# Kernel optimization log

Measured on AMD Instinct MI355X. Metric: run time of the kernel, lower is better.

## Reference

```python
import jax, jax.numpy as jnp
import numpy as np

B, C, H, W = 256, 2048, 16, 8
NUM_CLASSES = 10000
SCALE = 1.0  # cls_layer.s for cls_type='Linear', scale=1
N_ITERS = 20


def setup_inputs() -> dict:
    key = jax.random.key(0)
    k1, k2, k3 = jax.random.split(key, 3)
    features = jax.random.normal(k1, (B, C, H, W), dtype=jnp.float32)
    targets = jax.random.randint(k2, (B,), 0, NUM_CLASSES)
    # nn.init.normal_(self.weight, std=0.01)
    weight = jax.random.normal(k3, (NUM_CLASSES, C), dtype=jnp.float32) * 0.01
    return {"features": features, "targets": targets, "weight": weight}


def reference(features, targets, weight):
    # 1) GlobalAvgPool over H,W then squeeze -> [B, C]; bottleneck is identity
    #    (embedding_dim=0, with_bnneck=False).
    neck_feat = features.mean(axis=(2, 3))
    t = neck_feat.shape[0]

    # cls_type == 'Linear': logits = F.linear(neck_feat, weight); cls_layer is
    # a pass-through, so every loop iteration computes identical quantities
    # (the random 'maskarea' in the original is overwritten before use).
    logits = jnp.einsum('bc,nc->bn', neck_feat, weight)  # [B, num_classes]
    soft = jax.nn.softmax(logits, axis=1)

    # right_prob = softmax probability at the target class (scatter+mul+sum)
    right_prob = jnp.take_along_axis(soft, targets[:, None], axis=1)[:, 0]  # [t]

    # All N_ITERS iterations append the same right_prob, so at the final
    # iteration: mean == right_prob, variance over iterations == 0.
    mean_sl = right_prob                      # [t]
    var_sl = jnp.zeros_like(right_prob)       # [t]
    con = mean_sl / (var_sl * 1e4)            # -> +inf (matches torch div-by-0)
    ri = jnp.tanh(1.2 * con)                  # tanh(inf) = 1.0
    # new_weight[i] = t * ri[i] / ri.sum()
    new_weight = (t * ri / ri.sum())[None, :]  # [1, t]

    cls_outputs = logits                       # Linear cls layer is identity
    pred_class_logits = logits * SCALE
    feat = neck_feat                           # neck_feat == 'before', bottleneck identity
    return cls_outputs, pred_class_logits, feat, new_weight
```

## Files before the change

kernel.cpp:

```cpp
#include <hip/hip_runtime.h>


#define OUT1_OFF (256 * 10000)
#define FEAT_OFF (2 * 256 * 10000)
#define NW_OFF   (2 * 256 * 10000 + 256 * 2048)

typedef __attribute__((ext_vector_type(4))) float f32x4;
typedef __attribute__((ext_vector_type(8))) short bf16x8;
typedef __attribute__((ext_vector_type(4))) unsigned int u32x4;

__device__ inline unsigned pk2bf(float lo, float hi) {
    unsigned a = __float_as_uint(lo), b = __float_as_uint(hi);
    unsigned ra = (a + 0x7FFFu + ((a >> 16) & 1u)) >> 16;
    unsigned rb = (b + 0x7FFFu + ((b >> 16) & 1u)) & 0xFFFF0000u;
    return ra | rb;
}

__device__ inline void gload_lds16(const void* g, void* l) {
    __builtin_amdgcn_global_load_lds(
        (const __attribute__((address_space(1))) void*)g,
        (__attribute__((address_space(3))) void*)l, 16, 0, 0);
}

__global__ __launch_bounds__(256) void pool_kernel(
    const float* __restrict__ f, float* __restrict__ out,
    unsigned int* __restrict__ wsA32) {
    int tid = threadIdx.x;
    int g = tid >> 5;
    int l = tid & 31;
    int r0 = blockIdx.x * 16 + g * 2;
    const f32x4* s0 = (const f32x4*)(f + (size_t)r0 * 128);
    f32x4 v0 = s0[l];
    f32x4 v1 = s0[l + 32];
    float a = v0[0] + v0[1] + v0[2] + v0[3];
    float b = v1[0] + v1[1] + v1[2] + v1[3];
#pragma unroll
    for (int off = 16; off >= 1; off >>= 1) {
        a += __shfl_xor(a, off);
        b += __shfl_xor(b, off);
    }
    if (l == 0) {
        float m0 = a * (1.0f / 128.0f), m1 = b * (1.0f / 128.0f);
        float2 fv; fv.x = m0; fv.y = m1;
        *(float2*)&out[FEAT_OFF + r0] = fv;
        int bb = r0 >> 11, c = r0 & 2047;
        int chunk = ((bb >> 4) * 256 + (c >> 3)) * 16 + (bb & 15);
        wsA32[chunk * 4 + ((c & 7) >> 1)] = pk2bf(m0, m1);
    }
    if (blockIdx.x == 0) out[NW_OFF + tid] = 1.0f;
}

__global__ __launch_bounds__(512) void gemm_kernel(
    const u32x4* __restrict__ A16, const float* __restrict__ W,
    float* __restrict__ out) {
    __shared__ u32x4 As[3][2048];
    __shared__ u32x4 Bs[3][512];

    int tid = threadIdx.x;
    int n0 = blockIdx.x * 64;
    int wid = tid >> 6, lane = tid & 63;
    int wm = wid >> 1, wn = wid & 1;
    int r = lane & 15, kqu = lane >> 4;

    const u32x4* ga[4];
#pragma unroll
    for (int i = 0; i < 4; ++i) {
        int ci = tid + i * 512;
        ga[i] = A16 + (((ci >> 7) * 256 + ((ci >> 4) & 7)) * 16 + (ci & 15));
    }
    int nr = n0 + (((tid >> 7) << 4) | (tid & 15));
    if (nr > 9999) nr = 9999;
    int kg = (tid >> 4) & 7;
    const f32x4* gb = (const f32x4*)(W + (size_t)nr * 2048 + kg * 8);

    f32x4 acc[4][2];
#pragma unroll
    for (int i = 0; i < 4; ++i)
#pragma unroll
        for (int j = 0; j < 2; ++j) acc[i][j] = (f32x4){0.f, 0.f, 0.f, 0.f};

    f32x4 rbA0, rbA1, rbB0, rbB1;

#define STAGE_A(kt, buf)                                           \
    {                                                              \
        _Pragma("unroll") for (int i = 0; i < 4; ++i)              \
            gload_lds16(ga[i] + (kt) * 128, &As[buf][tid + i * 512]); \
    }
#define LOAD_B(kt, r0_, r1_)                \
    {                                       \
        r0_ = gb[(kt) * 16];                \
        r1_ = gb[(kt) * 16 + 1];            \
    }
#define PACK_B(buf, r0_, r1_)                              \
    {                                                      \
        u32x4 p;                                           \
        p.x = pk2bf(r0_[0], r0_[1]);                       \
        p.y = pk2bf(r0_[2], r0_[3]);                       \
        p.z = pk2bf(r1_[0], r1_[1]);                       \
        p.w = pk2bf(r1_[2], r1_[3]);                       \
        Bs[buf][tid] = p;                                  \
    }

    STAGE_A(0, 0); LOAD_B(0, rbA0, rbA1);
    STAGE_A(1, 1); LOAD_B(1, rbB0, rbB1);
    asm volatile("s_waitcnt vmcnt(6)" ::: "memory");
    __builtin_amdgcn_sched_barrier(0);
    PACK_B(0, rbA0, rbA1);
    asm volatile("s_waitcnt lgkmcnt(0)" ::: "memory");
    __builtin_amdgcn_sched_barrier(0);
    __builtin_amdgcn_s_barrier();
    __builtin_amdgcn_sched_barrier(0);

    for (int kt = 0; kt < 32; ++kt) {
        int cur = kt % 3;
        if (kt <= 29) {
            int nx2 = (kt + 2) % 3;
            STAGE_A(kt + 2, nx2);
            if (kt & 1) { LOAD_B(kt + 2, rbB0, rbB1); }
            else        { LOAD_B(kt + 2, rbA0, rbA1); }
        }
#pragma unroll
        for (int ks = 0; ks < 2; ++ks) {
            int kcl = ks * 4 + kqu;
            bf16x8 av[4], bv[2];
#pragma unroll
            for (int i = 0; i < 4; ++i)
                av[i] = *(const bf16x8*)&As[cur][(wm * 4 + i) * 128 + kcl * 16 + r];
#pragma unroll
            for (int j = 0; j < 2; ++j)
                bv[j] = *(const bf16x8*)&Bs[cur][(wn * 2 + j) * 128 + kcl * 16 + r];
#pragma unroll
            for (int i = 0; i < 4; ++i)
#pragma unroll
                for (int j = 0; j < 2; ++j)
                    acc[i][j] = __builtin_amdgcn_mfma_f32_16x16x32_bf16(
                        av[i], bv[j], acc[i][j], 0, 0, 0);
        }
        if (kt <= 29) { asm volatile("s_waitcnt vmcnt(6)" ::: "memory"); }
        else          { asm volatile("s_waitcnt vmcnt(0)" ::: "memory"); }
        __builtin_amdgcn_sched_barrier(0);
        if (kt <= 30) {
            int nx1 = (kt + 1) % 3;
            if (kt & 1) { PACK_B(nx1, rbA0, rbA1); }
            else        { PACK_B(nx1, rbB0, rbB1); }
            asm volatile("s_waitcnt lgkmcnt(0)" ::: "memory");
            __builtin_amdgcn_sched_barrier(0);
            __builtin_amdgcn_s_barrier();
        }
        __builtin_amdgcn_sched_barrier(0);
    }

#pragma unroll
    for (int i = 0; i < 4; ++i)
#pragma unroll
        for (int j = 0; j < 2; ++j) {
            int n = n0 + (wn * 2 + j) * 16 + r;
            if (n < 10000) {
                int mbase = (wm * 4 + i) * 16 + kqu * 4;
#pragma unroll
                for (int q = 0; q < 4; ++q) {
                    float v = acc[i][j][q];
                    size_t off = (size_t)(mbase + q) * 10000 + n;
                    out[off] = v;
                    out[OUT1_OFF + off] = v;
                }
            }
        }
#undef STAGE_A
#undef LOAD_B
#undef PACK_B
}

extern "C" void kernel_launch(void* const* d_in, const int* in_sizes, int n_in,
                              void* d_out, int out_size, void* d_ws, size_t ws_size,
                              hipStream_t stream) {
    const float* feats = (const float*)d_in[0];
    const float* weight = (const float*)d_in[2];
    float* out = (float*)d_out;

    pool_kernel<<<32768, 256, 0, stream>>>(feats, out, (unsigned int*)d_ws);
    gemm_kernel<<<157, 512, 0, stream>>>((const u32x4*)d_ws, weight, out);
}
```

Before: 105.0 us.

## Split GEMM across M halves and coarsen pooling work per block

The GEMM grid now splits the 256-row M dimension into two halves, launching 314 blocks instead of 157 so more CUs on the device get work. Each block keeps a smaller A tile and fewer accumulators, at the cost of reading and bf16-converting the weight matrix twice. The pooling kernel now handles 256 rows per block over 8 iterations with 4 rows per group, using vectorized stores, which cuts the block count from 32768 to 2048.

```diff
diff --git a/kernel.cpp b/kernel.cpp
--- a/kernel.cpp
+++ b/kernel.cpp
@@ -28,24 +28,37 @@
     int tid = threadIdx.x;
     int g = tid >> 5;
     int l = tid & 31;
-    int r0 = blockIdx.x * 16 + g * 2;
-    const f32x4* s0 = (const f32x4*)(f + (size_t)r0 * 128);
-    f32x4 v0 = s0[l];
-    f32x4 v1 = s0[l + 32];
-    float a = v0[0] + v0[1] + v0[2] + v0[3];
-    float b = v1[0] + v1[1] + v1[2] + v1[3];
 #pragma unroll
-    for (int off = 16; off >= 1; off >>= 1) {
-        a += __shfl_xor(a, off);
-        b += __shfl_xor(b, off);
-    }
-    if (l == 0) {
-        float m0 = a * (1.0f / 128.0f), m1 = b * (1.0f / 128.0f);
-        float2 fv; fv.x = m0; fv.y = m1;
-        *(float2*)&out[FEAT_OFF + r0] = fv;
-        int bb = r0 >> 11, c = r0 & 2047;
-        int chunk = ((bb >> 4) * 256 + (c >> 3)) * 16 + (bb & 15);
-        wsA32[chunk * 4 + ((c & 7) >> 1)] = pk2bf(m0, m1);
+    for (int it = 0; it < 8; ++it) {
+        int r0 = blockIdx.x * 256 + it * 32 + g * 4;
+        const f32x4* s0 = (const f32x4*)(f + (size_t)r0 * 128);
+        f32x4 v0 = s0[l];
+        f32x4 v1 = s0[l + 32];
+        f32x4 v2 = s0[l + 64];
+        f32x4 v3 = s0[l + 96];
+        float a0 = v0[0] + v0[1] + v0[2] + v0[3];
+        float a1 = v1[0] + v1[1] + v1[2] + v1[3];
+        float a2 = v2[0] + v2[1] + v2[2] + v2[3];
+        float a3 = v3[0] + v3[1] + v3[2] + v3[3];
+#pragma unroll
+        for (int off = 16; off >= 1; off >>= 1) {
+            a0 += __shfl_xor(a0, off);
+            a1 += __shfl_xor(a1, off);
+            a2 += __shfl_xor(a2, off);
+            a3 += __shfl_xor(a3, off);
+        }
+        if (l == 0) {
+            float m0 = a0 * (1.0f / 128.0f), m1 = a1 * (1.0f / 128.0f);
+            float m2 = a2 * (1.0f / 128.0f), m3 = a3 * (1.0f / 128.0f);
+            f32x4 fv = {m0, m1, m2, m3};
+            *(f32x4*)&out[FEAT_OFF + r0] = fv;
+            int bb = r0 >> 11, c = r0 & 2047;
+            int chunk = ((bb >> 4) * 256 + (c >> 3)) * 16 + (bb & 15);
+            uint2 pw;
+            pw.x = pk2bf(m0, m1);
+            pw.y = pk2bf(m2, m3);
+            *(uint2*)&wsA32[chunk * 4 + ((c & 7) >> 1)] = pw;
+        }
     }
     if (blockIdx.x == 0) out[NW_OFF + tid] = 1.0f;
 }
@@ -53,57 +66,58 @@
 __global__ __launch_bounds__(512) void gemm_kernel(
     const u32x4* __restrict__ A16, const float* __restrict__ W,
     float* __restrict__ out) {
-    __shared__ u32x4 As[3][2048];
+    __shared__ u32x4 As[3][1024];
     __shared__ u32x4 Bs[3][512];
 
     int tid = threadIdx.x;
-    int n0 = blockIdx.x * 64;
+    int mhalf = blockIdx.x;
+    int n0 = blockIdx.y * 64;
     int wid = tid >> 6, lane = tid & 63;
     int wm = wid >> 1, wn = wid & 1;
     int r = lane & 15, kqu = lane >> 4;
 
-    const u32x4* ga[4];
+    const u32x4* ga[2];
 #pragma unroll
-    for (int i = 0; i < 4; ++i) {
+    for (int i = 0; i < 2; ++i) {
         int ci = tid + i * 512;
-        ga[i] = A16 + (((ci >> 7) * 256 + ((ci >> 4) & 7)) * 16 + (ci & 15));
+        ga[i] = A16 + (((mhalf * 8 + (ci >> 7)) * 256 + ((ci >> 4) & 7)) * 16 + (ci & 15));
     }
     int nr = n0 + (((tid >> 7) << 4) | (tid & 15));
     if (nr > 9999) nr = 9999;
     int kg = (tid >> 4) & 7;
     const f32x4* gb = (const f32x4*)(W + (size_t)nr * 2048 + kg * 8);
 
-    f32x4 acc[4][2];
+    f32x4 acc[2][2];
 #pragma unroll
-    for (int i = 0; i < 4; ++i)
+    for (int i = 0; i < 2; ++i)
 #pragma unroll
         for (int j = 0; j < 2; ++j) acc[i][j] = (f32x4){0.f, 0.f, 0.f, 0.f};
 
     f32x4 rbA0, rbA1, rbB0, rbB1;
 
-#define STAGE_A(kt, buf)                                           \
-    {                                                              \
-        _Pragma("unroll") for (int i = 0; i < 4; ++i)              \
+#define STAGE_A(kt, buf)                                              \
+    {                                                                 \
+        _Pragma("unroll") for (int i = 0; i < 2; ++i)                 \
             gload_lds16(ga[i] + (kt) * 128, &As[buf][tid + i * 512]); \
     }
-#define LOAD_B(kt, r0_, r1_)                \
-    {                                       \
-        r0_ = gb[(kt) * 16];                \
-        r1_ = gb[(kt) * 16 + 1];            \
+#define LOAD_B(kt, r0_, r1_)     \
+    {                            \
+        r0_ = gb[(kt) * 16];     \
+        r1_ = gb[(kt) * 16 + 1]; \
     }
-#define PACK_B(buf, r0_, r1_)                              \
-    {                                                      \
-        u32x4 p;                                           \
-        p.x = pk2bf(r0_[0], r0_[1]);                       \
-        p.y = pk2bf(r0_[2], r0_[3]);                       \
-        p.z = pk2bf(r1_[0], r1_[1]);                       \
-        p.w = pk2bf(r1_[2], r1_[3]);                       \
-        Bs[buf][tid] = p;                                  \
+#define PACK_B(buf, r0_, r1_)            \
+    {                                    \
+        u32x4 p;                         \
+        p.x = pk2bf(r0_[0], r0_[1]);     \
+        p.y = pk2bf(r0_[2], r0_[3]);     \
+        p.z = pk2bf(r1_[0], r1_[1]);     \
+        p.w = pk2bf(r1_[2], r1_[3]);     \
+        Bs[buf][tid] = p;                \
     }
 
     STAGE_A(0, 0); LOAD_B(0, rbA0, rbA1);
     STAGE_A(1, 1); LOAD_B(1, rbB0, rbB1);
-    asm volatile("s_waitcnt vmcnt(6)" ::: "memory");
+    asm volatile("s_waitcnt vmcnt(4)" ::: "memory");
     __builtin_amdgcn_sched_barrier(0);
     PACK_B(0, rbA0, rbA1);
     asm volatile("s_waitcnt lgkmcnt(0)" ::: "memory");
@@ -122,21 +136,21 @@
 #pragma unroll
         for (int ks = 0; ks < 2; ++ks) {
             int kcl = ks * 4 + kqu;
-            bf16x8 av[4], bv[2];
+            bf16x8 av[2], bv[2];
 #pragma unroll
-            for (int i = 0; i < 4; ++i)
-                av[i] = *(const bf16x8*)&As[cur][(wm * 4 + i) * 128 + kcl * 16 + r];
+            for (int i = 0; i < 2; ++i)
+                av[i] = *(const bf16x8*)&As[cur][(wm * 2 + i) * 128 + kcl * 16 + r];
 #pragma unroll
             for (int j = 0; j < 2; ++j)
                 bv[j] = *(const bf16x8*)&Bs[cur][(wn * 2 + j) * 128 + kcl * 16 + r];
 #pragma unroll
-            for (int i = 0; i < 4; ++i)
+            for (int i = 0; i < 2; ++i)
 #pragma unroll
                 for (int j = 0; j < 2; ++j)
                     acc[i][j] = __builtin_amdgcn_mfma_f32_16x16x32_bf16(
                         av[i], bv[j], acc[i][j], 0, 0, 0);
         }
-        if (kt <= 29) { asm volatile("s_waitcnt vmcnt(6)" ::: "memory"); }
+        if (kt <= 29) { asm volatile("s_waitcnt vmcnt(4)" ::: "memory"); }
         else          { asm volatile("s_waitcnt vmcnt(0)" ::: "memory"); }
         __builtin_amdgcn_sched_barrier(0);
         if (kt <= 30) {
@@ -151,12 +165,12 @@
     }
 
 #pragma unroll
-    for (int i = 0; i < 4; ++i)
+    for (int i = 0; i < 2; ++i)
 #pragma unroll
         for (int j = 0; j < 2; ++j) {
             int n = n0 + (wn * 2 + j) * 16 + r;
             if (n < 10000) {
-                int mbase = (wm * 4 + i) * 16 + kqu * 4;
+                int mbase = mhalf * 128 + (wm * 2 + i) * 16 + kqu * 4;
 #pragma unroll
                 for (int q = 0; q < 4; ++q) {
                     float v = acc[i][j][q];
@@ -178,6 +192,6 @@
     const float* weight = (const float*)d_in[2];
     float* out = (float*)d_out;
 
-    pool_kernel<<<32768, 256, 0, stream>>>(feats, out, (unsigned int*)d_ws);
-    gemm_kernel<<<157, 512, 0, stream>>>((const u32x4*)d_ws, weight, out);
+    pool_kernel<<<2048, 256, 0, stream>>>(feats, out, (unsigned int*)d_ws);
+    gemm_kernel<<<dim3(2, 157), 512, 0, stream>>>((const u32x4*)d_ws, weight, out);
 }
```

Result: slower. 115.4 us (+9.9%).

## Load GEMM operands directly into registers, dropping LDS staging and barriers

Applied to the files above, without the earlier changes.

The GEMM kernel no longer stages A and B tiles through shared memory with a triple-buffered pipeline and block barriers. Each wave now loads its own A fragments and fp32 W rows straight into registers, double-buffered across two register sets, and converts W to bf16 in registers just before the MFMAs. This is meant to remove LDS traffic and barrier stalls. In exchange, A fragments that were shared across waves in LDS are now fetched redundantly from global memory or cache, and register pressure rises substantially.

```diff
diff --git a/kernel.cpp b/kernel.cpp
--- a/kernel.cpp
+++ b/kernel.cpp
@@ -14,12 +14,6 @@
     unsigned ra = (a + 0x7FFFu + ((a >> 16) & 1u)) >> 16;
     unsigned rb = (b + 0x7FFFu + ((b >> 16) & 1u)) & 0xFFFF0000u;
     return ra | rb;
-}
-
-__device__ inline void gload_lds16(const void* g, void* l) {
-    __builtin_amdgcn_global_load_lds(
-        (const __attribute__((address_space(1))) void*)g,
-        (__attribute__((address_space(3))) void*)l, 16, 0, 0);
 }
 
 __global__ __launch_bounds__(256) void pool_kernel(
@@ -53,25 +47,21 @@
 __global__ __launch_bounds__(512) void gemm_kernel(
     const u32x4* __restrict__ A16, const float* __restrict__ W,
     float* __restrict__ out) {
-    __shared__ u32x4 As[3][2048];
-    __shared__ u32x4 Bs[3][512];
-
     int tid = threadIdx.x;
     int n0 = blockIdx.x * 64;
     int wid = tid >> 6, lane = tid & 63;
     int wm = wid >> 1, wn = wid & 1;
-    int r = lane & 15, kqu = lane >> 4;
+    int r = lane & 15, q = lane >> 4;
 
-    const u32x4* ga[4];
-#pragma unroll
-    for (int i = 0; i < 4; ++i) {
-        int ci = tid + i * 512;
-        ga[i] = A16 + (((ci >> 7) * 256 + ((ci >> 4) & 7)) * 16 + (ci & 15));
-    }
-    int nr = n0 + (((tid >> 7) << 4) | (tid & 15));
-    if (nr > 9999) nr = 9999;
-    int kg = (tid >> 4) & 7;
-    const f32x4* gb = (const f32x4*)(W + (size_t)nr * 2048 + kg * 8);
+    const u32x4* paBase = A16 + q * 16 + r;
+    int wmBase = wm * 16384;
+
+    int row0 = n0 + wn * 32 + r;
+    if (row0 > 9999) row0 = 9999;
+    int row1 = row0 + 16;
+    if (row1 > 9999) row1 = 9999;
+    const f32x4* pB0 = (const f32x4*)(W + (size_t)row0 * 2048) + q * 2;
+    const f32x4* pB1 = (const f32x4*)(W + (size_t)row1 * 2048) + q * 2;
 
     f32x4 acc[4][2];
 #pragma unroll
@@ -79,76 +69,73 @@
 #pragma unroll
         for (int j = 0; j < 2; ++j) acc[i][j] = (f32x4){0.f, 0.f, 0.f, 0.f};
 
-    f32x4 rbA0, rbA1, rbB0, rbB1;
+    u32x4 Xa0, Xa1, Xa2, Xa3, Xa4, Xa5, Xa6, Xa7;
+    f32x4 Xb0, Xb1, Xb2, Xb3, Xb4, Xb5, Xb6, Xb7;
+    u32x4 Ya0, Ya1, Ya2, Ya3, Ya4, Ya5, Ya6, Ya7;
+    f32x4 Yb0, Yb1, Yb2, Yb3, Yb4, Yb5, Yb6, Yb7;
 
-#define STAGE_A(kt, buf)                                           \
-    {                                                              \
-        _Pragma("unroll") for (int i = 0; i < 4; ++i)              \
-            gload_lds16(ga[i] + (kt) * 128, &As[buf][tid + i * 512]); \
-    }
-#define LOAD_B(kt, r0_, r1_)                \
-    {                                       \
-        r0_ = gb[(kt) * 16];                \
-        r1_ = gb[(kt) * 16 + 1];            \
-    }
-#define PACK_B(buf, r0_, r1_)                              \
-    {                                                      \
-        u32x4 p;                                           \
-        p.x = pk2bf(r0_[0], r0_[1]);                       \
-        p.y = pk2bf(r0_[2], r0_[3]);                       \
-        p.z = pk2bf(r1_[0], r1_[1]);                       \
-        p.w = pk2bf(r1_[2], r1_[3]);                       \
-        Bs[buf][tid] = p;                                  \
+#define ISSUE(S, kt)                                      \
+    {                                                     \
+        const u32x4* pa = paBase + (kt) * 128;            \
+        S##a0 = pa[wmBase];                               \
+        S##a1 = pa[wmBase + 64];                          \
+        S##a2 = pa[wmBase + 4096];                        \
+        S##a3 = pa[wmBase + 4160];                        \
+        S##a4 = pa[wmBase + 8192];                        \
+        S##a5 = pa[wmBase + 8256];                        \
+        S##a6 = pa[wmBase + 12288];                       \
+        S##a7 = pa[wmBase + 12352];                       \
+        S##b0 = pB0[(kt)*16];                             \
+        S##b1 = pB0[(kt)*16 + 1];                         \
+        S##b2 = pB0[(kt)*16 + 8];                         \
+        S##b3 = pB0[(kt)*16 + 9];                         \
+        S##b4 = pB1[(kt)*16];                             \
+        S##b5 = pB1[(kt)*16 + 1];                         \
+        S##b6 = pB1[(kt)*16 + 8];                         \
+        S##b7 = pB1[(kt)*16 + 9];                         \
     }
 
-    STAGE_A(0, 0); LOAD_B(0, rbA0, rbA1);
-    STAGE_A(1, 1); LOAD_B(1, rbB0, rbB1);
-    asm volatile("s_waitcnt vmcnt(6)" ::: "memory");
-    __builtin_amdgcn_sched_barrier(0);
-    PACK_B(0, rbA0, rbA1);
-    asm volatile("s_waitcnt lgkmcnt(0)" ::: "memory");
-    __builtin_amdgcn_sched_barrier(0);
-    __builtin_amdgcn_s_barrier();
-    __builtin_amdgcn_sched_barrier(0);
+#define CVT(bv, p0, p1)                  \
+    {                                    \
+        u32x4 t;                         \
+        t.x = pk2bf(p0[0], p0[1]);       \
+        t.y = pk2bf(p0[2], p0[3]);       \
+        t.z = pk2bf(p1[0], p1[1]);       \
+        t.w = pk2bf(p1[2], p1[3]);       \
+        bv = *(bf16x8*)&t;               \
+    }
 
-    for (int kt = 0; kt < 32; ++kt) {
-        int cur = kt % 3;
-        if (kt <= 29) {
-            int nx2 = (kt + 2) % 3;
-            STAGE_A(kt + 2, nx2);
-            if (kt & 1) { LOAD_B(kt + 2, rbB0, rbB1); }
-            else        { LOAD_B(kt + 2, rbA0, rbA1); }
-        }
-#pragma unroll
-        for (int ks = 0; ks < 2; ++ks) {
-            int kcl = ks * 4 + kqu;
-            bf16x8 av[4], bv[2];
-#pragma unroll
-            for (int i = 0; i < 4; ++i)
-                av[i] = *(const bf16x8*)&As[cur][(wm * 4 + i) * 128 + kcl * 16 + r];
-#pragma unroll
-            for (int j = 0; j < 2; ++j)
-                bv[j] = *(const bf16x8*)&Bs[cur][(wn * 2 + j) * 128 + kcl * 16 + r];
-#pragma unroll
-            for (int i = 0; i < 4; ++i)
-#pragma unroll
-                for (int j = 0; j < 2; ++j)
-                    acc[i][j] = __builtin_amdgcn_mfma_f32_16x16x32_bf16(
-                        av[i], bv[j], acc[i][j], 0, 0, 0);
-        }
-        if (kt <= 29) { asm volatile("s_waitcnt vmcnt(6)" ::: "memory"); }
-        else          { asm volatile("s_waitcnt vmcnt(0)" ::: "memory"); }
-        __builtin_amdgcn_sched_barrier(0);
-        if (kt <= 30) {
-            int nx1 = (kt + 1) % 3;
-            if (kt & 1) { PACK_B(nx1, rbA0, rbA1); }
-            else        { PACK_B(nx1, rbB0, rbB1); }
-            asm volatile("s_waitcnt lgkmcnt(0)" ::: "memory");
-            __builtin_amdgcn_sched_barrier(0);
-            __builtin_amdgcn_s_barrier();
-        }
-        __builtin_amdgcn_sched_barrier(0);
+#define MF(i, a_, bv, j)                                       \
+    acc[i][j] = __builtin_amdgcn_mfma_f32_16x16x32_bf16(       \
+        *(bf16x8*)&a_, bv, acc[i][j], 0, 0, 0)
+
+#define COMPUTE(S)                                                          \
+    {                                                                       \
+        bf16x8 bv;                                                          \
+        CVT(bv, S##b0, S##b1);                                \
+        MF(0, S##a0, bv, 0); MF(1, S##a2, bv, 0);                           \
+        MF(2, S##a4, bv, 0); MF(3, S##a6, bv, 0);                           \
+        CVT(bv, S##b2, S##b3);                                \
+        MF(0, S##a1, bv, 0); MF(1, S##a3, bv, 0);                           \
+        MF(2, S##a5, bv, 0); MF(3, S##a7, bv, 0);                           \
+        CVT(bv, S##b4, S##b5);                                \
+        MF(0, S##a0, bv, 1); MF(1, S##a2, bv, 1);                           \
+        MF(2, S##a4, bv, 1); MF(3, S##a6, bv, 1);                           \
+        CVT(bv, S##b6, S##b7);                                \
+        MF(0, S##a1, bv, 1); MF(1, S##a3, bv, 1);                           \
+        MF(2, S##a5, bv, 1); MF(3, S##a7, bv, 1);                           \
     }
+
+    ISSUE(X, 0);
+    ISSUE(Y, 1);
+    for (int kt = 0; kt < 30; kt += 2) {
+        COMPUTE(X);
+        ISSUE(X, kt + 2);
+        COMPUTE(Y);
+        ISSUE(Y, kt + 3);
+    }
+    COMPUTE(X);
+    COMPUTE(Y);
 
 #pragma unroll
     for (int i = 0; i < 4; ++i)
@@ -156,19 +143,20 @@
         for (int j = 0; j < 2; ++j) {
             int n = n0 + (wn * 2 + j) * 16 + r;
             if (n < 10000) {
-                int mbase = (wm * 4 + i) * 16 + kqu * 4;
+                int mbase = (wm * 4 + i) * 16 + q * 4;
 #pragma unroll
-                for (int q = 0; q < 4; ++q) {
-                    float v = acc[i][j][q];
-                    size_t off = (size_t)(mbase + q) * 10000 + n;
+                for (int qq = 0; qq < 4; ++qq) {
+                    float v = acc[i][j][qq];
+                    size_t off = (size_t)(mbase + qq) * 10000 + n;
                     out[off] = v;
                     out[OUT1_OFF + off] = v;
                 }
             }
         }
-#undef STAGE_A
-#undef LOAD_B
-#undef PACK_B
+#undef ISSUE
+#undef CVT
+#undef MF
+#undef COMPUTE
 }
 
 extern "C" void kernel_launch(void* const* d_in, const int* in_sizes, int n_in,
```

Measured after the change: 128.2 us. 1.22x slower.
